# Kernel tuning notes

Hardware: AMD Instinct MI355X
Metric: run time of the kernel (lower is better)

Reference implementation:

```python
import jax, jax.numpy as jnp
import numpy as np

B, S, H, I, E, TOP_K = 2, 1024, 1024, 2048, 8, 2


def setup_inputs() -> dict:
    key = jax.random.key(0)
    k1, k2, k3, k4 = jax.random.split(key, 4)
    return {
        "hidden_states": jax.random.normal(k1, (B, S, H), dtype=jnp.float32),
        "gate_weight": jax.random.normal(k2, (E, H), dtype=jnp.float32) * 0.02,
        "gate_up_proj": jax.random.normal(k3, (E, 2 * I, H), dtype=jnp.float32) * 0.02,
        "down_proj": jax.random.normal(k4, (E, H, I), dtype=jnp.float32) * 0.02,
    }


def reference(hidden_states, gate_weight, gate_up_proj, down_proj):
    b, s, h = hidden_states.shape
    T = b * s
    x = hidden_states.reshape(T, h)

    # --- router ---
    router_logits = x @ gate_weight.T                          # [T, E]
    router_probs = jax.nn.softmax(router_logits.astype(jnp.float32), axis=-1)
    router_probs = router_probs.astype(router_logits.dtype)
    top_vals, top_idx = jax.lax.top_k(router_probs, TOP_K)     # [T, K]
    # norm_topk_prob = True
    routing_weights = top_vals / jnp.maximum(top_vals.sum(-1, keepdims=True), 1e-12)

    # --- dense all-expert FFN ---
    gu = jnp.einsum('th,eoh->eto', x, gate_up_proj)            # [E, T, 2I]
    gate_h, up_h = jnp.split(gu, 2, axis=-1)
    inter = jax.nn.silu(gate_h) * up_h                          # [E, T, I]
    expert_out = jnp.einsum('eti,ehi->eth', inter, down_proj).astype(jnp.float32)  # [E, T, H]

    # --- pairwise Frobenius similarity (sim = 1 - dist/max_dist, diag=1) ---
    flat = expert_out.reshape(E, -1)
    gram = flat @ flat.T                                        # [E, E]
    sq = jnp.diagonal(gram)
    dist = jnp.sqrt(jnp.clip(sq[:, None] + sq[None, :] - 2.0 * gram, 0.0))
    dist = dist.at[jnp.arange(E), jnp.arange(E)].set(0.0)
    sim = 1.0 - dist / jnp.maximum(dist.max(), 1e-12)
    sim = sim.at[jnp.arange(E), jnp.arange(E)].set(1.0)

    # --- top-k weighted combine (gather along expert axis) ---
    gathered = expert_out[top_idx, jnp.arange(T)[:, None]]      # [T, K, H]
    final = (gathered * routing_weights[..., None].astype(jnp.float32)).sum(axis=1)
    final = final.astype(hidden_states.dtype).reshape(b, s, h)
    return final, sim
```

## Files before the change

kernel.cpp:

```cpp
#include <hip/hip_runtime.h>
#include <math.h>

#define T_TOK 2048
#define H_DIM 1024
#define I_DIM 2048
#define NEXP  8

typedef _Float16 f16x8 __attribute__((ext_vector_type(8)));
typedef _Float16 f16x4 __attribute__((ext_vector_type(4)));
typedef float    f32x4 __attribute__((ext_vector_type(4)));

__device__ __forceinline__ void cp16(const void* g, void* l) {
  __builtin_amdgcn_global_load_lds(
      (const __attribute__((address_space(1))) void*)g,
      (__attribute__((address_space(3))) void*)l, 16, 0, 0);
}

__global__ __launch_bounds__(256) void cvt_f16_kernel(
    const float* __restrict__ in, _Float16* __restrict__ hi, int n) {
  int i = (blockIdx.x * 256 + threadIdx.x) * 4;
  if (i >= n) return;
  float4 v = *(const float4*)(in + i);
  f16x4 hv = {(_Float16)v.x, (_Float16)v.y, (_Float16)v.z, (_Float16)v.w};
  *(f16x4*)(hi + i) = hv;
}

__global__ __launch_bounds__(256) void prep_kernel(
    const float* __restrict__ x, _Float16* __restrict__ xHi,
    const float* __restrict__ gup, _Float16* __restrict__ gup16,
    const float* __restrict__ dwn, _Float16* __restrict__ wd16,
    const float* __restrict__ gw,
    int* __restrict__ topIdx, float* __restrict__ topW,
    float* __restrict__ gram) {
  const int b = blockIdx.x;
  const int tid = threadIdx.x;

  if (b < 512) {
    if (b == 0 && tid < 36) gram[tid] = 0.f;
    const int wave = tid >> 6, lane = tid & 63;
    const int t = b * 4 + wave;
    float p[NEXP];
#pragma unroll
    for (int e = 0; e < NEXP; ++e) p[e] = 0.f;
    const float* xr = x + (size_t)t * H_DIM;
    for (int h = lane; h < H_DIM; h += 64) {
      float xv = xr[h];
#pragma unroll
      for (int e = 0; e < NEXP; ++e) p[e] += xv * gw[e * H_DIM + h];
    }
#pragma unroll
    for (int e = 0; e < NEXP; ++e) {
      float v = p[e];
      for (int off = 32; off > 0; off >>= 1) v += __shfl_down(v, off);
      p[e] = v;
    }
    if (lane == 0) {
      float mx = p[0];
#pragma unroll
      for (int e = 1; e < NEXP; ++e) mx = fmaxf(mx, p[e]);
      float ex[NEXP], s = 0.f;
#pragma unroll
      for (int e = 0; e < NEXP; ++e) { ex[e] = expf(p[e] - mx); s += ex[e]; }
#pragma unroll
      for (int e = 0; e < NEXP; ++e) ex[e] /= s;
      int i0 = 0; float v0 = ex[0];
#pragma unroll
      for (int e = 1; e < NEXP; ++e) if (ex[e] > v0) { v0 = ex[e]; i0 = e; }
      int i1 = -1; float v1 = -1.f;
#pragma unroll
      for (int e = 0; e < NEXP; ++e) if (e != i0 && ex[e] > v1) { v1 = ex[e]; i1 = e; }
      float sum = fmaxf(v0 + v1, 1e-12f);
      topIdx[2 * t] = i0;  topIdx[2 * t + 1] = i1;
      topW[2 * t] = v0 / sum;  topW[2 * t + 1] = v1 / sum;
    }
    return;
  }

  int rb = b - 512;
  const float* src;
  _Float16* dst;
  if (rb < 2048) {
    src = x;  dst = xHi;
  } else if (rb < 2048 + 32768) {
    rb -= 2048;  src = gup;  dst = gup16;
  } else {
    rb -= (2048 + 32768);  src = dwn;  dst = wd16;
  }
  const size_t i = (size_t)rb * 1024 + (size_t)tid * 4;
  float4 v = *(const float4*)(src + i);
  f16x4 hv = {(_Float16)v.x, (_Float16)v.y, (_Float16)v.z, (_Float16)v.w};
  *(f16x4*)(dst + i) = hv;
}

__global__ __launch_bounds__(256, 2) void gemm_gateup(
    const _Float16* __restrict__ xHi, const _Float16* __restrict__ gup16,
    _Float16* __restrict__ intHi) {
  __shared__ _Float16 lds[24576];

  const int tid = threadIdx.x;
  const int wave = tid >> 6, lane = tid & 63;
  const int rowA0 = blockIdx.y * 128;
  const int colB0 = blockIdx.x * 128;
  const int e = blockIdx.z;

  const int sr = lane >> 3;
  const int sc = lane & 7;
  const int gcol = (sc ^ sr) * 8;
  const int rbase = wave * 8 + sr;

  const int wm = wave >> 1, wn = wave & 1;
  const int fr = lane & 15;
  const int quad = lane >> 4;

  f32x4 accG[4][4], accU[4][4];
#pragma unroll
  for (int i = 0; i < 4; ++i)
#pragma unroll
    for (int j = 0; j < 4; ++j) {
      accG[i][j] = (f32x4){0.f, 0.f, 0.f, 0.f};
      accU[i][j] = (f32x4){0.f, 0.f, 0.f, 0.f};
    }

  const _Float16* gupG = gup16 + ((size_t)e * 2 * I_DIM + colB0) * H_DIM;
  const _Float16* gupU = gupG + (size_t)I_DIM * H_DIM;
  char* ldsB = (char*)lds;

  for (int k0 = 0; k0 < H_DIM; k0 += 64) {
    const int kcol = k0 + gcol;
#pragma unroll
    for (int i = 0; i < 4; ++i) {
      const int row = i * 32 + rbase;
      const unsigned dst = (unsigned)(i * 4096 + wave * 1024);
      cp16(xHi  + (size_t)(rowA0 + row) * H_DIM + kcol, ldsB + dst);
      cp16(gupG + (size_t)row * H_DIM + kcol, ldsB + 16384u + dst);
      cp16(gupU + (size_t)row * H_DIM + kcol, ldsB + 32768u + dst);
    }
    __syncthreads();

#pragma unroll
    for (int kk = 0; kk < 2; ++kk) {
      f16x8 ah[4];
#pragma unroll
      for (int i = 0; i < 4; ++i) {
        const int row = wm * 64 + i * 16 + fr;
        ah[i] = *(const f16x8*)&lds[row * 64 + (((kk * 4 + quad) ^ (fr & 7)) * 8)];
      }
#pragma unroll
      for (int j = 0; j < 4; ++j) {
        const int row = wn * 64 + j * 16 + fr;
        const int boff = row * 64 + (((kk * 4 + quad) ^ (fr & 7)) * 8);
        f16x8 bg = *(const f16x8*)&lds[8192 + boff];
        f16x8 bu = *(const f16x8*)&lds[16384 + boff];
#pragma unroll
        for (int i = 0; i < 4; ++i) {
          accG[i][j] = __builtin_amdgcn_mfma_f32_16x16x32_f16(ah[i], bg, accG[i][j], 0, 0, 0);
          accU[i][j] = __builtin_amdgcn_mfma_f32_16x16x32_f16(ah[i], bu, accU[i][j], 0, 0, 0);
        }
      }
    }
    __syncthreads();
  }

  const int er = quad * 4;
  const int ec = lane & 15;
#pragma unroll
  for (int i = 0; i < 4; ++i)
#pragma unroll
    for (int j = 0; j < 4; ++j) {
      const int row = rowA0 + wm * 64 + i * 16 + er;
      const int col = colB0 + wn * 64 + j * 16 + ec;
#pragma unroll
      for (int r = 0; r < 4; ++r) {
        float g = accG[i][j][r], u = accU[i][j][r];
        float val = g / (1.f + __expf(-g)) * u;
        intHi[((size_t)e * T_TOK + row + r) * I_DIM + col] = (_Float16)val;
      }
    }
}

__global__ __launch_bounds__(512, 2) void gemm_down(
    const _Float16* __restrict__ intHi, const _Float16* __restrict__ wd16,
    _Float16* __restrict__ eo) {
  __shared__ _Float16 lds[65536];

  const int tid = threadIdx.x;
  const int wave = tid >> 6, lane = tid & 63;
  const int rowA0 = blockIdx.x * 256;
  const int colB0 = blockIdx.y * 256;
  const int e = blockIdx.z;

  const int sr = lane >> 3;
  const int sc = lane & 7;
  const int gcol = (sc ^ sr) * 8;

  const int wm = wave >> 2;
  const int wn = wave & 3;
  const int fr = lane & 15;
  const int quad = lane >> 4;

  f32x4 acc[8][4];
#pragma unroll
  for (int i = 0; i < 8; ++i)
#pragma unroll
    for (int j = 0; j < 4; ++j) acc[i][j] = (f32x4){0.f, 0.f, 0.f, 0.f};

  const _Float16* aSrc = intHi + (size_t)e * T_TOK * I_DIM +
                         (size_t)(rowA0 + wave * 8 + sr) * I_DIM + gcol;
  const _Float16* bSrc = wd16 + ((size_t)e * H_DIM + colB0 + wave * 8 + sr) * I_DIM + gcol;
  char* ldsB = (char*)lds;
  char* ldsAw = ldsB + wave * 1024u;
  char* ldsBw = ldsAw + 32768u;

  const int NT = I_DIM / 64;

#pragma unroll
  for (int s = 0; s < 4; ++s) {
    cp16(aSrc + (size_t)s * 64 * I_DIM, ldsAw + s * 8192u);
    cp16(bSrc + (size_t)s * 64 * I_DIM, ldsBw + s * 8192u);
  }
  __syncthreads();

  for (int t = 0; t < NT; ++t) {
    const int cur = t & 1;
    if (t < NT - 1) {
      const unsigned nb = (unsigned)((cur ^ 1) * 65536u);
      const _Float16* aS = aSrc + (size_t)(t + 1) * 64;
      const _Float16* bS = bSrc + (size_t)(t + 1) * 64;
#pragma unroll
      for (int s = 0; s < 4; ++s) {
        cp16(aS + (size_t)s * 64 * I_DIM, ldsAw + nb + s * 8192u);
        cp16(bS + (size_t)s * 64 * I_DIM, ldsBw + nb + s * 8192u);
      }
    }
    const int cb = cur * 32768;
#pragma unroll
    for (int ks = 0; ks < 2; ++ks) {
      const int ksl = (ks * 4 + quad);
      f16x8 bh[4];
#pragma unroll
      for (int j = 0; j < 4; ++j) {
        const int row = wn * 64 + j * 16 + fr;
        bh[j] = *(const f16x8*)&lds[cb + 16384 + row * 64 + ((ksl ^ (fr & 7)) * 8)];
      }
      f16x8 ah[8];
#pragma unroll
      for (int i = 0; i < 8; ++i) {
        const int row = wm * 128 + i * 16 + fr;
        ah[i] = *(const f16x8*)&lds[cb + row * 64 + ((ksl ^ (fr & 7)) * 8)];
      }
      __builtin_amdgcn_s_setprio(1);
#pragma unroll
      for (int j = 0; j < 4; ++j)
#pragma unroll
        for (int i = 0; i < 8; ++i)
          acc[i][j] = __builtin_amdgcn_mfma_f32_16x16x32_f16(ah[i], bh[j], acc[i][j], 0, 0, 0);
      __builtin_amdgcn_s_setprio(0);
    }
    __syncthreads();
  }

  const int er = quad * 4;
  const int ec = lane & 15;
#pragma unroll
  for (int i = 0; i < 8; ++i)
#pragma unroll
    for (int j = 0; j < 4; ++j) {
      const int row = rowA0 + wm * 128 + i * 16 + er;
      const int col = colB0 + wn * 64 + j * 16 + ec;
#pragma unroll
      for (int r = 0; r < 4; ++r)
        eo[((size_t)e * T_TOK + row + r) * H_DIM + col] = (_Float16)acc[i][j][r];
    }
}

__global__ __launch_bounds__(256) void gram_kernel(
    const _Float16* __restrict__ eo, float* __restrict__ gram) {
  float s[36];
#pragma unroll
  for (int p = 0; p < 36; ++p) s[p] = 0.f;
  const size_t total = (size_t)T_TOK * H_DIM;
  const size_t stride = (size_t)gridDim.x * 256;
  for (size_t j = (size_t)blockIdx.x * 256 + threadIdx.x; j < total; j += stride) {
    float v[NEXP];
#pragma unroll
    for (int e = 0; e < NEXP; ++e) v[e] = (float)eo[(size_t)e * total + j];
    int p = 0;
#pragma unroll
    for (int a = 0; a < NEXP; ++a)
#pragma unroll
      for (int b = a; b < NEXP; ++b) { s[p] += v[a] * v[b]; ++p; }
  }
#pragma unroll
  for (int p = 0; p < 36; ++p) {
    float v = s[p];
    for (int off = 32; off > 0; off >>= 1) v += __shfl_down(v, off);
    s[p] = v;
  }
  __shared__ float red[4][36];
  const int wave = threadIdx.x >> 6, lane = threadIdx.x & 63;
  if (lane == 0)
#pragma unroll
    for (int p = 0; p < 36; ++p) red[wave][p] = s[p];
  __syncthreads();
  if (threadIdx.x < 36) {
    float v = red[0][threadIdx.x] + red[1][threadIdx.x] + red[2][threadIdx.x] + red[3][threadIdx.x];
    atomicAdd(&gram[threadIdx.x], v);
  }
}

__global__ __launch_bounds__(256) void final_kernel(
    const _Float16* __restrict__ eo, const int* __restrict__ topIdx,
    const float* __restrict__ topW, const float* __restrict__ gram,
    float* __restrict__ out) {
  const int t = blockIdx.x;
  if (t == T_TOK) {
    if (threadIdx.x < 64) {
      const int q = threadIdx.x;
      const int e1 = q >> 3, e2 = q & 7;
      int a = e1 < e2 ? e1 : e2;
      int b = e1 < e2 ? e2 : e1;
      const float g = gram[a * 8 - a * (a - 1) / 2 + (b - a)];
      const float sq1 = gram[e1 * 8 - e1 * (e1 - 1) / 2];
      const float sq2 = gram[e2 * 8 - e2 * (e2 - 1) / 2];
      float d2 = fmaxf(sq1 + sq2 - 2.f * g, 0.f);
      float dist = (e1 == e2) ? 0.f : sqrtf(d2);
      float dmax = dist;
      for (int off = 32; off > 0; off >>= 1) dmax = fmaxf(dmax, __shfl_xor(dmax, off));
      float sim = 1.f - dist / fmaxf(dmax, 1e-12f);
      if (e1 == e2) sim = 1.f;
      out[(size_t)T_TOK * H_DIM + q] = sim;
    }
    return;
  }
  const int c = threadIdx.x * 4;
  const int i0 = topIdx[2 * t], i1 = topIdx[2 * t + 1];
  const float w0 = topW[2 * t], w1 = topW[2 * t + 1];
  const size_t per = (size_t)T_TOK * H_DIM;
  f16x4 a = *(const f16x4*)&eo[(size_t)i0 * per + (size_t)t * H_DIM + c];
  f16x4 b = *(const f16x4*)&eo[(size_t)i1 * per + (size_t)t * H_DIM + c];
  float4 r;
  r.x = w0 * (float)a[0] + w1 * (float)b[0];
  r.y = w0 * (float)a[1] + w1 * (float)b[1];
  r.z = w0 * (float)a[2] + w1 * (float)b[2];
  r.w = w0 * (float)a[3] + w1 * (float)b[3];
  *(float4*)&out[(size_t)t * H_DIM + c] = r;
}

extern "C" void kernel_launch(void* const* d_in, const int* in_sizes, int n_in,
                              void* d_out, int out_size, void* d_ws, size_t ws_size,
                              hipStream_t stream) {
  (void)in_sizes; (void)n_in; (void)out_size;
  const float* x   = (const float*)d_in[0];
  const float* gw  = (const float*)d_in[1];
  const float* gup = (const float*)d_in[2];
  const float* dwn = (const float*)d_in[3];
  float* out = (float*)d_out;

  char* ws = (char*)d_ws;
  const size_t MB = 1u << 20;
  _Float16* xHi    = (_Float16*)(ws + 0 * MB);
  _Float16* intHi  = (_Float16*)(ws + 4 * MB);
  _Float16* gup16  = (_Float16*)(ws + 68 * MB);
  _Float16* eo     = (_Float16*)(ws + 100 * MB);
  int*      topIdx = (int*)(ws + 132 * MB);
  float*    topW   = (float*)(ws + 132 * MB + 16384);
  float*    gram   = (float*)(ws + 132 * MB + 32768);

  const int doDwn = ws_size >= (size_t)169 * MB;
  _Float16* wd16 = doDwn ? (_Float16*)(ws + 136 * MB)
                         : (_Float16*)(ws + 68 * MB);

  const int prepBlocks = 512 + 2048 + 32768 + (doDwn ? 16384 : 0);
  prep_kernel<<<prepBlocks, 256, 0, stream>>>(
      x, xHi, gup, gup16, dwn, wd16, gw, topIdx, topW, gram);

  gemm_gateup<<<dim3(I_DIM / 128, T_TOK / 128, NEXP), 256, 0, stream>>>(
      xHi, gup16, intHi);

  if (!doDwn)
    cvt_f16_kernel<<<16384, 256, 0, stream>>>(dwn, wd16, NEXP * H_DIM * I_DIM);

  gemm_down<<<dim3(T_TOK / 256, H_DIM / 256, NEXP), 512, 0, stream>>>(
      intHi, wd16, eo);

  gram_kernel<<<2048, 256, 0, stream>>>(eo, gram);
  final_kernel<<<T_TOK + 1, 256, 0, stream>>>(eo, topIdx, topW, gram, out);
}
```

Measured before the change: 499.3 us.

## Shrink down-proj GEMM tile, drop double buffering, vectorize gram loads

The down-projection GEMM goes from 256x256 tiles with double-buffered LDS to 128x256 tiles with a single LDS buffer. It also raises the launch-bounds occupancy hint from 2 to 4 and doubles the grid along the token axis. The aim is more resident blocks and waves to hide latency, in place of explicit software prefetching, at the cost of less reuse per tile and a stall on each K step. The gram kernel now loads eight f16 values per expert per thread with vector loads and runs half as many blocks, to cut load instruction count.

```diff
diff --git a/kernel.cpp b/kernel.cpp
--- a/kernel.cpp
+++ b/kernel.cpp
@@ -178,14 +178,14 @@
     }
 }
 
-__global__ __launch_bounds__(512, 2) void gemm_down(
+__global__ __launch_bounds__(512, 4) void gemm_down(
     const _Float16* __restrict__ intHi, const _Float16* __restrict__ wd16,
     _Float16* __restrict__ eo) {
-  __shared__ _Float16 lds[65536];
+  __shared__ _Float16 lds[24576];
 
   const int tid = threadIdx.x;
   const int wave = tid >> 6, lane = tid & 63;
-  const int rowA0 = blockIdx.x * 256;
+  const int rowA0 = blockIdx.x * 128;
   const int colB0 = blockIdx.y * 256;
   const int e = blockIdx.z;
 
@@ -198,9 +198,9 @@
   const int fr = lane & 15;
   const int quad = lane >> 4;
 
-  f32x4 acc[8][4];
-#pragma unroll
-  for (int i = 0; i < 8; ++i)
+  f32x4 acc[4][4];
+#pragma unroll
+  for (int i = 0; i < 4; ++i)
 #pragma unroll
     for (int j = 0; j < 4; ++j) acc[i][j] = (f32x4){0.f, 0.f, 0.f, 0.f};
 
@@ -208,53 +208,33 @@
                          (size_t)(rowA0 + wave * 8 + sr) * I_DIM + gcol;
   const _Float16* bSrc = wd16 + ((size_t)e * H_DIM + colB0 + wave * 8 + sr) * I_DIM + gcol;
   char* ldsB = (char*)lds;
-  char* ldsAw = ldsB + wave * 1024u;
-  char* ldsBw = ldsAw + 32768u;
-
-  const int NT = I_DIM / 64;
-
-#pragma unroll
-  for (int s = 0; s < 4; ++s) {
-    cp16(aSrc + (size_t)s * 64 * I_DIM, ldsAw + s * 8192u);
-    cp16(bSrc + (size_t)s * 64 * I_DIM, ldsBw + s * 8192u);
-  }
-  __syncthreads();
-
-  for (int t = 0; t < NT; ++t) {
-    const int cur = t & 1;
-    if (t < NT - 1) {
-      const unsigned nb = (unsigned)((cur ^ 1) * 65536u);
-      const _Float16* aS = aSrc + (size_t)(t + 1) * 64;
-      const _Float16* bS = bSrc + (size_t)(t + 1) * 64;
-#pragma unroll
-      for (int s = 0; s < 4; ++s) {
-        cp16(aS + (size_t)s * 64 * I_DIM, ldsAw + nb + s * 8192u);
-        cp16(bS + (size_t)s * 64 * I_DIM, ldsBw + nb + s * 8192u);
-      }
-    }
-    const int cb = cur * 32768;
-#pragma unroll
-    for (int ks = 0; ks < 2; ++ks) {
-      const int ksl = (ks * 4 + quad);
-      f16x8 bh[4];
+
+  for (int k0 = 0; k0 < I_DIM; k0 += 64) {
+#pragma unroll
+    for (int c = 0; c < 2; ++c)
+      cp16(aSrc + (size_t)c * 64 * I_DIM + k0, ldsB + c * 8192u + wave * 1024u);
+#pragma unroll
+    for (int c = 0; c < 4; ++c)
+      cp16(bSrc + (size_t)c * 64 * I_DIM + k0, ldsB + 16384u + c * 8192u + wave * 1024u);
+    __syncthreads();
+
+#pragma unroll
+    for (int kk = 0; kk < 2; ++kk) {
+      const int ksl = kk * 4 + quad;
+      f16x8 ah[4];
+#pragma unroll
+      for (int i = 0; i < 4; ++i) {
+        const int row = wm * 64 + i * 16 + fr;
+        ah[i] = *(const f16x8*)&lds[row * 64 + ((ksl ^ (fr & 7)) * 8)];
+      }
 #pragma unroll
       for (int j = 0; j < 4; ++j) {
         const int row = wn * 64 + j * 16 + fr;
-        bh[j] = *(const f16x8*)&lds[cb + 16384 + row * 64 + ((ksl ^ (fr & 7)) * 8)];
-      }
-      f16x8 ah[8];
-#pragma unroll
-      for (int i = 0; i < 8; ++i) {
-        const int row = wm * 128 + i * 16 + fr;
-        ah[i] = *(const f16x8*)&lds[cb + row * 64 + ((ksl ^ (fr & 7)) * 8)];
-      }
-      __builtin_amdgcn_s_setprio(1);
-#pragma unroll
-      for (int j = 0; j < 4; ++j)
-#pragma unroll
-        for (int i = 0; i < 8; ++i)
-          acc[i][j] = __builtin_amdgcn_mfma_f32_16x16x32_f16(ah[i], bh[j], acc[i][j], 0, 0, 0);
-      __builtin_amdgcn_s_setprio(0);
+        f16x8 bh = *(const f16x8*)&lds[8192 + row * 64 + ((ksl ^ (fr & 7)) * 8)];
+#pragma unroll
+        for (int i = 0; i < 4; ++i)
+          acc[i][j] = __builtin_amdgcn_mfma_f32_16x16x32_f16(ah[i], bh, acc[i][j], 0, 0, 0);
+      }
     }
     __syncthreads();
   }
@@ -262,10 +242,10 @@
   const int er = quad * 4;
   const int ec = lane & 15;
 #pragma unroll
-  for (int i = 0; i < 8; ++i)
+  for (int i = 0; i < 4; ++i)
 #pragma unroll
     for (int j = 0; j < 4; ++j) {
-      const int row = rowA0 + wm * 128 + i * 16 + er;
+      const int row = rowA0 + wm * 64 + i * 16 + er;
       const int col = colB0 + wn * 64 + j * 16 + ec;
 #pragma unroll
       for (int r = 0; r < 4; ++r)
@@ -279,16 +259,22 @@
 #pragma unroll
   for (int p = 0; p < 36; ++p) s[p] = 0.f;
   const size_t total = (size_t)T_TOK * H_DIM;
-  const size_t stride = (size_t)gridDim.x * 256;
-  for (size_t j = (size_t)blockIdx.x * 256 + threadIdx.x; j < total; j += stride) {
-    float v[NEXP];
-#pragma unroll
-    for (int e = 0; e < NEXP; ++e) v[e] = (float)eo[(size_t)e * total + j];
-    int p = 0;
-#pragma unroll
-    for (int a = 0; a < NEXP; ++a)
-#pragma unroll
-      for (int b = a; b < NEXP; ++b) { s[p] += v[a] * v[b]; ++p; }
+  const size_t stride = (size_t)gridDim.x * 256 * 8;
+  for (size_t j = ((size_t)blockIdx.x * 256 + threadIdx.x) * 8; j < total; j += stride) {
+    f16x8 ve[NEXP];
+#pragma unroll
+    for (int e = 0; e < NEXP; ++e) ve[e] = *(const f16x8*)&eo[(size_t)e * total + j];
+#pragma unroll
+    for (int k = 0; k < 8; ++k) {
+      float v[NEXP];
+#pragma unroll
+      for (int e = 0; e < NEXP; ++e) v[e] = (float)ve[e][k];
+      int p = 0;
+#pragma unroll
+      for (int a = 0; a < NEXP; ++a)
+#pragma unroll
+        for (int b = a; b < NEXP; ++b) { s[p] += v[a] * v[b]; ++p; }
+    }
   }
 #pragma unroll
   for (int p = 0; p < 36; ++p) {
@@ -380,9 +366,9 @@
   if (!doDwn)
     cvt_f16_kernel<<<16384, 256, 0, stream>>>(dwn, wd16, NEXP * H_DIM * I_DIM);
 
-  gemm_down<<<dim3(T_TOK / 256, H_DIM / 256, NEXP), 512, 0, stream>>>(
+  gemm_down<<<dim3(T_TOK / 128, H_DIM / 256, NEXP), 512, 0, stream>>>(
       intHi, wd16, eo);
 
-  gram_kernel<<<2048, 256, 0, stream>>>(eo, gram);
+  gram_kernel<<<1024, 256, 0, stream>>>(eo, gram);
   final_kernel<<<T_TOK + 1, 256, 0, stream>>>(eo, topIdx, topW, gram, out);
 }
```

New measurement: 491.3 us. About the same (-1.6%).
